# Performance work log

Measured on AMD Instinct MI355X. Metric: run time of the kernel, lower is better.

The kernel has to match this reference:

```python
import jax, jax.numpy as jnp
import numpy as np

BRANCH, DEPTH = 10, 3          # balanced hierarchy: 10^3 = 1000 leaf classes
NUM_CLASSES = BRANCH ** DEPTH
NUM_EDGES = DEPTH
N_TOKENS = 32768
IGNORE_INDEX = -100


def _build_tree_tensors():
    """Reproduce HierarchicalLLLoss.__init__ for a balanced tree.

    For leaf i, its ancestor edge at level j (j=0 is the leaf's own edge)
    spans the contiguous leaf block of size BRANCH**j containing i.
    """
    C, E = NUM_CLASSES, NUM_EDGES
    onehot_num = np.zeros((C, C, E), np.float32)
    onehot_den = np.zeros((C, C, E), np.float32)
    weights = np.zeros((C, E), np.float32)
    leaves = np.arange(C)
    cols = np.arange(C)
    for j in range(E):
        s_num = BRANCH ** j
        start_num = (leaves // s_num) * s_num              # [C]
        mask_num = (cols[None, :] >= start_num[:, None]) & (cols[None, :] < (start_num + s_num)[:, None])
        onehot_num[:, :, j] = mask_num.astype(np.float32)
        s_den = BRANCH ** (j + 1)                          # parent subtree; top level -> all ones
        start_den = (leaves // s_den) * s_den
        mask_den = (cols[None, :] >= start_den[:, None]) & (cols[None, :] < (start_den + s_den)[:, None])
        onehot_den[:, :, j] = mask_den.astype(np.float32)
        weights[:, j] = np.exp(-0.5 * j)                   # edge weight by height above leaf
    return onehot_num, onehot_den, weights


def setup_inputs() -> dict:
    key = jax.random.key(0)
    k1, k2 = jax.random.split(key)
    onehot_num, onehot_den, weights = _build_tree_tensors()
    # class "probabilities" (positive; normalization cancels in the num/den ratio)
    inputs = jax.random.uniform(k1, (N_TOKENS, NUM_CLASSES), jnp.float32, 1e-4, 1.0)
    target = jax.random.randint(k2, (N_TOKENS,), 0, NUM_CLASSES, dtype=jnp.int64)
    return {
        "inputs": inputs,
        "target": target,
        "onehot_num": jnp.asarray(onehot_num),
        "onehot_den": jnp.asarray(onehot_den),
        "weights": jnp.asarray(weights),
    }


def reference(inputs, target, onehot_num, onehot_den, weights):
    valid = target != IGNORE_INDEX                          # [N] bool
    t = jnp.where(valid, target, 0)                          # safe gather index
    # bmm of [N,1,C] with gathered [N,C,E] -> [N,E]
    num = jnp.einsum("nc,nce->ne", inputs, onehot_num[t])
    den = jnp.einsum("nc,nce->ne", inputs, onehot_den[t])
    nz = num != 0
    num = jnp.where(nz, -jnp.log(num / jnp.where(nz, den, 1.0)), num)
    # flip does not change the sum but is kept for fidelity to the source
    per_tok = jnp.sum(jnp.flip(weights[t] * num, axis=1), axis=1)  # [N]
    per_tok = jnp.where(valid, per_tok, 0.0)
    count = jnp.maximum(jnp.sum(valid.astype(jnp.float32)), 1.0)
    return jnp.sum(per_tok) / count
```

## Files before the change

kernel.cpp:

```cpp
#include <hip/hip_runtime.h>
#include <math.h>

#define N_TOKENS     32768
#define NUM_CLASSES  1000
#define IGNORE_INDEX (-100)
#define WAVES_PER_BLK 4
#define NBLOCKS      (N_TOKENS / WAVES_PER_BLK)

template <int Ctrl>
__device__ __forceinline__ float dpp_add(float x) {
    const int v = __builtin_amdgcn_update_dpp(
        0, __float_as_int(x), Ctrl, 0xf, 0xf, true);
    return x + __int_as_float(v);
}
__device__ __forceinline__ float wave_sum(float x) {
    x = dpp_add<0x111>(x);
    x = dpp_add<0x112>(x);
    x = dpp_add<0x114>(x);
    x = dpp_add<0x118>(x);
    x = dpp_add<0x142>(x);
    x = dpp_add<0x143>(x);
    return x;
}

__global__ __launch_bounds__(256) void hll_main(
    const float* __restrict__ inputs,
    const int*   __restrict__ target,
    const float* __restrict__ weights,
    float2* __restrict__ partials)
{
    const int wave = threadIdx.x >> 6;
    const int lane = threadIdx.x & 63;
    const int n = blockIdx.x * WAVES_PER_BLK + wave;

    const int t = target[n];
    const bool valid = (t != IGNORE_INDEX);
    const int tt = valid ? t : 0;

    const float* __restrict__ rowp = inputs + (size_t)n * NUM_CLASSES;
    const float4* __restrict__ row = (const float4*)rowp;

    const float4 v0 = row[lane];
    const float4 v1 = row[lane + 64];
    const float4 v2 = row[lane + 128];
    float4 v3 = make_float4(0.f, 0.f, 0.f, 0.f);
    if (lane < 58) v3 = row[lane + 192];

    const int lo1  = (tt / 10) * 10;
    const int q2lo = (tt / 100) * 25;

    const float s0 = rowp[tt];
    const float w0 = weights[tt * 3 + 0];
    const float w1 = weights[tt * 3 + 1];
    const float w2 = weights[tt * 3 + 2];

    float s3 = 0.f, s2 = 0.f, s1 = 0.f;
    {
        const float4 vs[4] = {v0, v1, v2, v3};
        #pragma unroll
        for (int i = 0; i < 4; ++i) {
            const int idx4 = lane + 64 * i;
            const float4 v = vs[i];
            const float q = (v.x + v.y) + (v.z + v.w);
            s3 += q;
            s2 += ((unsigned)(idx4 - q2lo) < 25u) ? q : 0.f;
            const int c = idx4 * 4;
            s1 += ((unsigned)(c + 0 - lo1) < 10u) ? v.x : 0.f;
            s1 += ((unsigned)(c + 1 - lo1) < 10u) ? v.y : 0.f;
            s1 += ((unsigned)(c + 2 - lo1) < 10u) ? v.z : 0.f;
            s1 += ((unsigned)(c + 3 - lo1) < 10u) ? v.w : 0.f;
        }
    }

    s3 = wave_sum(s3);
    s2 = wave_sum(s2);
    s1 = wave_sum(s1);

    if (lane == 63) {
        float loss = 0.f;
        if (valid) {
            const float l0 = (s0 != 0.f) ? -logf(s0 / s1) : 0.f;
            const float l1 = (s1 != 0.f) ? -logf(s1 / s2) : 0.f;
            const float l2 = (s2 != 0.f) ? -logf(s2 / s3) : 0.f;
            loss = w0 * l0 + w1 * l1 + w2 * l2;
        }
        partials[n] = make_float2(loss, valid ? 1.f : 0.f);
    }
}

__global__ __launch_bounds__(256) void hll_final(
    const float4* __restrict__ p4,
    float* __restrict__ out)
{
    const int wave = threadIdx.x >> 6;
    const int lane = threadIdx.x & 63;
    float s = 0.f, c = 0.f;
    for (int i = threadIdx.x; i < N_TOKENS / 2; i += 256) {
        const float4 v = p4[i];
        s += v.x + v.z;
        c += v.y + v.w;
    }
    s = wave_sum(s);
    c = wave_sum(c);
    __shared__ float ss[4], sc[4];
    if (lane == 63) { ss[wave] = s; sc[wave] = c; }
    __syncthreads();
    if (threadIdx.x == 0) {
        const float S  = (ss[0] + ss[1]) + (ss[2] + ss[3]);
        const float Ct = (sc[0] + sc[1]) + (sc[2] + sc[3]);
        out[0] = S / fmaxf(Ct, 1.0f);
    }
}

extern "C" void kernel_launch(void* const* d_in, const int* in_sizes, int n_in,
                              void* d_out, int out_size, void* d_ws, size_t ws_size,
                              hipStream_t stream) {
    const float* inputs  = (const float*)d_in[0];
    const int*   target  = (const int*)d_in[1];
    const float* weights = (const float*)d_in[4];
    float* out = (float*)d_out;

    float2* partials = (float2*)d_ws;

    hll_main<<<NBLOCKS, 256, 0, stream>>>(inputs, target, weights, partials);
    hll_final<<<1, 256, 0, stream>>>((const float4*)partials, out);
}
```

Baseline: 215.8 us.

## Process two tokens per wave and reduce partials per block

Each wave now handles two token rows, issuing all loads for both up front to raise memory-level parallelism. The level-1 and level-2 sums are computed from small targeted reloads of the relevant contiguous ranges instead of masked accumulation over the full row. Per-block partials are combined through shared memory, shrinking the final kernel's input. DPP reductions are replaced with shuffle-down reductions, which may cost more instructions, and the extra targeted loads add some traffic that should hit in cache.

```diff
diff --git a/kernel.cpp b/kernel.cpp
--- a/kernel.cpp
+++ b/kernel.cpp
@@ -5,23 +5,8 @@
 #define NUM_CLASSES  1000
 #define IGNORE_INDEX (-100)
 #define WAVES_PER_BLK 4
-#define NBLOCKS      (N_TOKENS / WAVES_PER_BLK)
-
-template <int Ctrl>
-__device__ __forceinline__ float dpp_add(float x) {
-    const int v = __builtin_amdgcn_update_dpp(
-        0, __float_as_int(x), Ctrl, 0xf, 0xf, true);
-    return x + __int_as_float(v);
-}
-__device__ __forceinline__ float wave_sum(float x) {
-    x = dpp_add<0x111>(x);
-    x = dpp_add<0x112>(x);
-    x = dpp_add<0x114>(x);
-    x = dpp_add<0x118>(x);
-    x = dpp_add<0x142>(x);
-    x = dpp_add<0x143>(x);
-    return x;
-}
+#define TOK_PER_WAVE 2
+#define NBLOCKS      (N_TOKENS / (WAVES_PER_BLK * TOK_PER_WAVE))
 
 __global__ __launch_bounds__(256) void hll_main(
     const float* __restrict__ inputs,
@@ -31,60 +16,90 @@
 {
     const int wave = threadIdx.x >> 6;
     const int lane = threadIdx.x & 63;
-    const int n = blockIdx.x * WAVES_PER_BLK + wave;
+    const int n0 = (blockIdx.x * WAVES_PER_BLK + wave) * TOK_PER_WAVE;
+    const int n1 = n0 + 1;
 
-    const int t = target[n];
-    const bool valid = (t != IGNORE_INDEX);
-    const int tt = valid ? t : 0;
+    const float* __restrict__ rowpA = inputs + (size_t)n0 * NUM_CLASSES;
+    const float* __restrict__ rowpB = inputs + (size_t)n1 * NUM_CLASSES;
+    const float4* __restrict__ rowA = (const float4*)rowpA;
+    const float4* __restrict__ rowB = (const float4*)rowpB;
 
-    const float* __restrict__ rowp = inputs + (size_t)n * NUM_CLASSES;
-    const float4* __restrict__ row = (const float4*)rowp;
+    const float4 a0 = rowA[lane];
+    const float4 a1 = rowA[lane + 64];
+    const float4 a2 = rowA[lane + 128];
+    float4 a3 = make_float4(0.f, 0.f, 0.f, 0.f);
+    if (lane < 58) a3 = rowA[lane + 192];
+    const float4 b0 = rowB[lane];
+    const float4 b1 = rowB[lane + 64];
+    const float4 b2 = rowB[lane + 128];
+    float4 b3 = make_float4(0.f, 0.f, 0.f, 0.f);
+    if (lane < 58) b3 = rowB[lane + 192];
 
-    const float4 v0 = row[lane];
-    const float4 v1 = row[lane + 64];
-    const float4 v2 = row[lane + 128];
-    float4 v3 = make_float4(0.f, 0.f, 0.f, 0.f);
-    if (lane < 58) v3 = row[lane + 192];
+    const int tA = target[n0];
+    const int tB = target[n1];
+    const bool validA = (tA != IGNORE_INDEX);
+    const bool validB = (tB != IGNORE_INDEX);
+    const int ttA = validA ? tA : 0;
+    const int ttB = validB ? tB : 0;
 
-    const int lo1  = (tt / 10) * 10;
-    const int q2lo = (tt / 100) * 25;
+    float4 vs2A = make_float4(0.f, 0.f, 0.f, 0.f);
+    float4 vs2B = make_float4(0.f, 0.f, 0.f, 0.f);
+    if (lane < 25) {
+        vs2A = rowA[(ttA / 100) * 25 + lane];
+        vs2B = rowB[(ttB / 100) * 25 + lane];
+    }
+    float s1A = (lane < 10) ? rowpA[(ttA / 10) * 10 + lane] : 0.f;
+    float s1B = (lane < 10) ? rowpB[(ttB / 10) * 10 + lane] : 0.f;
+    const float s0A = rowpA[ttA];
+    const float s0B = rowpB[ttB];
 
-    const float s0 = rowp[tt];
-    const float w0 = weights[tt * 3 + 0];
-    const float w1 = weights[tt * 3 + 1];
-    const float w2 = weights[tt * 3 + 2];
+    float s3A = ((a0.x + a0.y) + (a0.z + a0.w)) + ((a1.x + a1.y) + (a1.z + a1.w))
+              + ((a2.x + a2.y) + (a2.z + a2.w)) + ((a3.x + a3.y) + (a3.z + a3.w));
+    float s3B = ((b0.x + b0.y) + (b0.z + b0.w)) + ((b1.x + b1.y) + (b1.z + b1.w))
+              + ((b2.x + b2.y) + (b2.z + b2.w)) + ((b3.x + b3.y) + (b3.z + b3.w));
+    float s2A = (vs2A.x + vs2A.y) + (vs2A.z + vs2A.w);
+    float s2B = (vs2B.x + vs2B.y) + (vs2B.z + vs2B.w);
 
-    float s3 = 0.f, s2 = 0.f, s1 = 0.f;
-    {
-        const float4 vs[4] = {v0, v1, v2, v3};
-        #pragma unroll
-        for (int i = 0; i < 4; ++i) {
-            const int idx4 = lane + 64 * i;
-            const float4 v = vs[i];
-            const float q = (v.x + v.y) + (v.z + v.w);
-            s3 += q;
-            s2 += ((unsigned)(idx4 - q2lo) < 25u) ? q : 0.f;
-            const int c = idx4 * 4;
-            s1 += ((unsigned)(c + 0 - lo1) < 10u) ? v.x : 0.f;
-            s1 += ((unsigned)(c + 1 - lo1) < 10u) ? v.y : 0.f;
-            s1 += ((unsigned)(c + 2 - lo1) < 10u) ? v.z : 0.f;
-            s1 += ((unsigned)(c + 3 - lo1) < 10u) ? v.w : 0.f;
-        }
+    #pragma unroll
+    for (int off = 32; off >= 1; off >>= 1) {
+        s3A += __shfl_down(s3A, off, 64);
+        s3B += __shfl_down(s3B, off, 64);
+        s2A += __shfl_down(s2A, off, 64);
+        s2B += __shfl_down(s2B, off, 64);
+        s1A += __shfl_down(s1A, off, 64);
+        s1B += __shfl_down(s1B, off, 64);
     }
 
-    s3 = wave_sum(s3);
-    s2 = wave_sum(s2);
-    s1 = wave_sum(s1);
-
-    if (lane == 63) {
-        float loss = 0.f;
-        if (valid) {
-            const float l0 = (s0 != 0.f) ? -logf(s0 / s1) : 0.f;
-            const float l1 = (s1 != 0.f) ? -logf(s1 / s2) : 0.f;
-            const float l2 = (s2 != 0.f) ? -logf(s2 / s3) : 0.f;
-            loss = w0 * l0 + w1 * l1 + w2 * l2;
+    __shared__ float rl[WAVES_PER_BLK], rc[WAVES_PER_BLK];
+    if (lane == 0) {
+        float loss = 0.f, cnt = 0.f;
+        if (validA) {
+            const float w0 = weights[ttA * 3 + 0];
+            const float w1 = weights[ttA * 3 + 1];
+            const float w2 = weights[ttA * 3 + 2];
+            const float l0 = (s0A != 0.f) ? -logf(s0A / s1A) : 0.f;
+            const float l1 = (s1A != 0.f) ? -logf(s1A / s2A) : 0.f;
+            const float l2 = (s2A != 0.f) ? -logf(s2A / s3A) : 0.f;
+            loss += w0 * l0 + w1 * l1 + w2 * l2;
+            cnt += 1.f;
         }
-        partials[n] = make_float2(loss, valid ? 1.f : 0.f);
+        if (validB) {
+            const float w0 = weights[ttB * 3 + 0];
+            const float w1 = weights[ttB * 3 + 1];
+            const float w2 = weights[ttB * 3 + 2];
+            const float l0 = (s0B != 0.f) ? -logf(s0B / s1B) : 0.f;
+            const float l1 = (s1B != 0.f) ? -logf(s1B / s2B) : 0.f;
+            const float l2 = (s2B != 0.f) ? -logf(s2B / s3B) : 0.f;
+            loss += w0 * l0 + w1 * l1 + w2 * l2;
+            cnt += 1.f;
+        }
+        rl[wave] = loss;
+        rc[wave] = cnt;
+    }
+    __syncthreads();
+    if (threadIdx.x == 0) {
+        partials[blockIdx.x] = make_float2((rl[0] + rl[1]) + (rl[2] + rl[3]),
+                                           (rc[0] + rc[1]) + (rc[2] + rc[3]));
     }
 }
 
@@ -95,15 +110,18 @@
     const int wave = threadIdx.x >> 6;
     const int lane = threadIdx.x & 63;
     float s = 0.f, c = 0.f;
-    for (int i = threadIdx.x; i < N_TOKENS / 2; i += 256) {
+    for (int i = threadIdx.x; i < NBLOCKS / 2; i += 256) {
         const float4 v = p4[i];
         s += v.x + v.z;
         c += v.y + v.w;
     }
-    s = wave_sum(s);
-    c = wave_sum(c);
+    #pragma unroll
+    for (int off = 32; off >= 1; off >>= 1) {
+        s += __shfl_down(s, off, 64);
+        c += __shfl_down(c, off, 64);
+    }
     __shared__ float ss[4], sc[4];
-    if (lane == 63) { ss[wave] = s; sc[wave] = c; }
+    if (lane == 0) { ss[wave] = s; sc[wave] = c; }
     __syncthreads();
     if (threadIdx.x == 0) {
         const float S  = (ss[0] + ss[1]) + (ss[2] + ss[3]);
```

Result: faster. 203.1 us (-5.9%).
